# Performance work log

Measured on AMD Instinct MI355X. Metric: run time of the kernel, lower is better.

## Reference

```python
import jax, jax.numpy as jnp
import numpy as np

B, T, V, NIMG = 128, 512, 128, 1000
E, IMG_E, H = 128, 32, 1024


def setup_inputs() -> dict:
    key = jax.random.key(0)
    ks = jax.random.split(key, 10)
    s = 0.02
    input_img = jax.random.randint(ks[0], (B,), 0, NIMG)
    x = jax.random.randint(ks[1], (B, T), 0, V)
    label = jax.random.randint(ks[2], (B, T), 0, V)
    emb_img = jax.random.normal(ks[3], (NIMG, IMG_E), dtype=jnp.float32) * s
    emb_char = jax.random.normal(ks[4], (V, E), dtype=jnp.float32) * s
    emb_char = emb_char.at[0].set(0.0)  # padding_idx row zeroed, pad id = 0
    W_proj = jax.random.normal(ks[5], (E, IMG_E + E), dtype=jnp.float32) * s
    b_proj = jnp.zeros((E,), jnp.float32)
    W_ih = jax.random.normal(ks[6], (4 * H, E), dtype=jnp.float32) * s
    W_hh = jax.random.normal(ks[7], (4 * H, H), dtype=jnp.float32) * s
    b_ih = jnp.zeros((4 * H,), jnp.float32)
    b_hh = jnp.zeros((4 * H,), jnp.float32)
    W_fc = jax.random.normal(ks[8], (V, H), dtype=jnp.float32) * s
    b_fc = jnp.zeros((V,), jnp.float32)
    return dict(input_img=input_img, x=x, label=label, emb_img=emb_img,
                emb_char=emb_char, W_proj=W_proj, b_proj=b_proj,
                W_ih=W_ih, W_hh=W_hh, b_ih=b_ih, b_hh=b_hh,
                W_fc=W_fc, b_fc=b_fc)


def _forward(input_img, x, label, emb_img, emb_char, W_proj, b_proj,
             W_ih, W_hh, b_ih, b_hh, W_fc, b_fc):
    # Teacher-forced token stream: step 0 uses x[:,0], step t uses label[:,t-1]
    tok = jnp.concatenate([x[:, :1], label[:, :-1]], axis=1)          # [B,T]
    img_e = emb_img[input_img]                                        # [B,IMG_E]
    tok_e = emb_char[tok]                                             # [B,T,E]
    b, t = tok_e.shape[0], tok_e.shape[1]
    cat = jnp.concatenate(
        [jnp.broadcast_to(img_e[:, None, :], (b, t, img_e.shape[1])), tok_e],
        axis=-1)                                                      # [B,T,IMG_E+E]
    inp = jnp.einsum('btc,ec->bte', cat, W_proj) + b_proj             # [B,T,E]
    # Precompute input-to-gate projection for all timesteps (one big GEMM)
    gates_x = jnp.einsum('bte,ge->btg', inp, W_ih) + b_ih + b_hh      # [B,T,4H]
    Hh = W_hh.shape[1]

    def step(carry, gx):
        h, c = carry
        g = gx + h @ W_hh.T                                           # [B,4H]
        i, f, gg, o = jnp.split(g, 4, axis=-1)                        # torch order i,f,g,o
        c = jax.nn.sigmoid(f) * c + jax.nn.sigmoid(i) * jnp.tanh(gg)
        h = jax.nn.sigmoid(o) * jnp.tanh(c)
        return (h, c), h

    h0 = jnp.zeros((b, Hh), inp.dtype)
    (_, _), hs = jax.lax.scan(step, (h0, h0), jnp.swapaxes(gates_x, 0, 1))
    hs = jnp.swapaxes(hs, 0, 1)                                       # [B,T,H]
    logits = jnp.einsum('bth,vh->btv', hs, W_fc) + b_fc               # [B,T,V]
    return logits


def reference(input_img, x, label, emb_img, emb_char, W_proj, b_proj,
              W_ih, W_hh, b_ih, b_hh, W_fc, b_fc):
    logits = _forward(input_img, x, label, emb_img, emb_char, W_proj, b_proj,
                      W_ih, W_hh, b_ih, b_hh, W_fc, b_fc)
    preds = jnp.argmax(logits, axis=-1)                               # [B,T]
    return logits, preds
```

## Files before the change

kernel.cpp:

```cpp
#include <hip/hip_runtime.h>
#include <hip/hip_cooperative_groups.h>
#include <cmath>

#define TSTEPS 512
#define BB     128
#define HD     1024
#define GD     4096
#define VD     128
#define ED     128
#define IE     32
#define CD     160

#define DPPMOV(v, ctrl) \
    __int_as_float(__builtin_amdgcn_update_dpp(0, __float_as_int(v), (ctrl), 0xF, 0xF, true))
#define DPP_XOR7  0x141
#define DPP_XOR1  0x0B1
#define DPP_XOR2  0x04E
#define DPP_XOR8  0x128


__global__ void fold_wc_kernel(const float* __restrict__ W_ih,
                               const float* __restrict__ W_proj,
                               const float* __restrict__ b_proj,
                               const float* __restrict__ b_ih,
                               const float* __restrict__ b_hh,
                               float* __restrict__ Wc,
                               float* __restrict__ gb) {
    int idx = blockIdx.x * 256 + threadIdx.x;
    if (idx < GD * CD) {
        int g = idx / CD, c = idx - g * CD;
        const float* wr = W_ih + g * ED;
        float s = 0.f;
        #pragma unroll 8
        for (int e = 0; e < ED; ++e) s = fmaf(wr[e], W_proj[e * CD + c], s);
        Wc[idx] = s;
    }
    if (idx < GD) {
        const float* wr = W_ih + idx * ED;
        float s = b_ih[idx] + b_hh[idx];
        #pragma unroll 8
        for (int e = 0; e < ED; ++e) s = fmaf(wr[e], b_proj[e], s);
        gb[idx] = s;
    }
}

__global__ void fold_gimg_kernel(const float* __restrict__ emb_img,
                                 const int* __restrict__ input_img,
                                 const float* __restrict__ Wc,
                                 const float* __restrict__ gb,
                                 float* __restrict__ Gimgb) {
    int idx = blockIdx.x * 256 + threadIdx.x;
    int b = idx >> 12, g = idx & (GD - 1);
    const float* e = emb_img + (size_t)input_img[b] * IE;
    const float* w = Wc + g * CD;
    float s = gb[g];
    #pragma unroll
    for (int k = 0; k < IE; ++k) s = fmaf(e[k], w[k], s);
    Gimgb[idx] = s;
}

__global__ void fold_gtok_kernel(const float* __restrict__ emb_char,
                                 const float* __restrict__ Wc,
                                 float* __restrict__ Gtok) {
    int idx = blockIdx.x * 256 + threadIdx.x;
    int v = idx >> 12, g = idx & (GD - 1);
    const float* e = emb_char + v * ED;
    const float* w = Wc + g * CD + IE;
    float s = 0.f;
    #pragma unroll 8
    for (int k = 0; k < ED; ++k) s = fmaf(e[k], w[k], s);
    Gtok[idx] = s;
}

__global__ void init_kernel(const int* __restrict__ x,
                            const int* __restrict__ label,
                            int* __restrict__ tokseq,
                            float* __restrict__ hbuf,
                            unsigned* __restrict__ barcnt) {
    int idx = blockIdx.x * 256 + threadIdx.x;
    if (idx < 2 * BB * HD) hbuf[idx] = 0.f;
    if (idx < TSTEPS * BB) {
        int t = idx >> 7, b = idx & (BB - 1);
        tokseq[idx] = (t == 0) ? x[b * TSTEPS] : label[b * TSTEPS + t - 1];
    }
    if (idx < 128) barcnt[idx] = 0;
}

__global__ __launch_bounds__(1024, 4) void lstm_fused(
    const float* __restrict__ W_hh,
    const float* __restrict__ Gimgb,
    const float* __restrict__ Gtok,
    const float* __restrict__ Wfc,
    const float* __restrict__ bfc,
    const int*   __restrict__ tokseq,
    float*       __restrict__ hbuf,
    float*       __restrict__ logits,
    unsigned*    __restrict__ barcnt)
{
    __shared__ float4 hlds4[16 * 256];

    const int tid  = threadIdx.x;
    const int bid  = blockIdx.x;
    const int bgrp = bid >> 6;
    const int jgrp = bid & 63;
    const int w    = tid >> 6;
    const int L    = tid & 63;
    const int col  = jgrp * 16 + w;
    const int lrow = L & 31;
    const int row_own = bgrp * 32 + lrow;
    const int pcap = (L >> 3) & 3;
    const bool b0 = (L & 1), b1 = ((L >> 1) & 1), b2 = ((L >> 2) & 1);

    const int kc = L & 31;
    const int v  = jgrp * 2 + (L >> 5);
    const float bfcv = bfc[v];

    const float4* __restrict__ Whh4 = reinterpret_cast<const float4*>(W_hh);
    const float4* __restrict__ Wfc4 = reinterpret_cast<const float4*>(Wfc);

    float4 wreg[4][4];
    #pragma unroll
    for (int g = 0; g < 4; ++g)
        #pragma unroll
        for (int i = 0; i < 4; ++i)
            wreg[g][i] = Whh4[(size_t)(g * HD + col) * 256 + i * 64 + L];

    #pragma unroll
    for (int g = 0; g < 4; ++g)
        #pragma unroll
        for (int i = 0; i < 4; ++i)
            asm volatile("" : "+v"(wreg[g][i].x), "+v"(wreg[g][i].y),
                              "+v"(wreg[g][i].z), "+v"(wreg[g][i].w));

    unsigned* cnt = barcnt + bgrp * 32;

    float ab0, ab1, ab2, ab3;
    {
        const int tok = tokseq[row_own];
        const float* gi = Gimgb + (size_t)row_own * GD + col;
        const float* gt = Gtok  + (size_t)tok     * GD + col;
        ab0 = gi[0]    + gt[0];
        ab1 = gi[1024] + gt[1024];
        ab2 = gi[2048] + gt[2048];
        ab3 = gi[3072] + gt[3072];
    }

    float c_reg = 0.f;
    int cur = 0;

    #pragma unroll 1
    for (int t = 0; t <= TSTEPS; ++t) {
        const bool last = (t == TSTEPS);
        float aval0 = 0.f, aval1 = 0.f, aval2 = 0.f, aval3 = 0.f;

        const float4* hsrc = reinterpret_cast<const float4*>(
            hbuf + (size_t)cur * (BB * HD));

        #pragma unroll 1
        for (int st = 0; st < 2; ++st) {
            {
                const float4* src = hsrc + (size_t)(bgrp * 32 + st * 16) * 256;
                #pragma unroll
                for (int j = 0; j < 4; ++j)
                    hlds4[tid + j * 1024] = src[tid + j * 1024];
            }
            __syncthreads();

            if (t > 0) {
                float s = 0.f;
                #pragma unroll
                for (int m = 0; m < 8; ++m) {
                    float4 h4 = hlds4[w * 256 + m * 32 + kc];
                    float4 w4 = Wfc4[(size_t)v * 256 + m * 32 + kc];
                    s = fmaf(h4.x, w4.x, fmaf(h4.y, w4.y,
                        fmaf(h4.z, w4.z, fmaf(h4.w, w4.w, s))));
                }
                s += __shfl_xor(s, 1);  s += __shfl_xor(s, 2);
                s += __shfl_xor(s, 4);  s += __shfl_xor(s, 8);
                s += __shfl_xor(s, 16);
                if (kc == 0)
                    logits[((size_t)(bgrp * 32 + st * 16 + w) * TSTEPS
                            + (t - 1)) * VD + v] = s + bfcv;
            }

            if (!last) {
                #pragma unroll 1
                for (int p = 0; p < 2; ++p) {
                    float acc[4][8];
                    #pragma unroll
                    for (int g = 0; g < 4; ++g)
                        #pragma unroll
                        for (int r = 0; r < 8; ++r) acc[g][r] = 0.f;

                    #pragma unroll
                    for (int r = 0; r < 8; ++r) {
                        const int rl = p * 8 + r;
                        #pragma unroll
                        for (int i = 0; i < 4; ++i) {
                            float4 h4 = hlds4[rl * 256 + i * 64 + L];
                            #pragma unroll
                            for (int g = 0; g < 4; ++g)
                                acc[g][r] = fmaf(wreg[g][i].x, h4.x,
                                             fmaf(wreg[g][i].y, h4.y,
                                              fmaf(wreg[g][i].z, h4.z,
                                               fmaf(wreg[g][i].w, h4.w,
                                                    acc[g][r]))));
                        }
                    }

                    const bool own = (pcap == st * 2 + p);
                    #pragma unroll
                    for (int g = 0; g < 4; ++g) {
                        float m0 = b2 ? acc[g][4] : acc[g][0];
                        float s0 = b2 ? acc[g][0] : acc[g][4];
                        float m1 = b2 ? acc[g][5] : acc[g][1];
                        float s1 = b2 ? acc[g][1] : acc[g][5];
                        float m2 = b2 ? acc[g][6] : acc[g][2];
                        float s2 = b2 ? acc[g][2] : acc[g][6];
                        float m3 = b2 ? acc[g][7] : acc[g][3];
                        float s3 = b2 ? acc[g][3] : acc[g][7];
                        float n0 = m0 + DPPMOV(s0, DPP_XOR7);
                        float n1 = m1 + DPPMOV(s1, DPP_XOR7);
                        float n2 = m2 + DPPMOV(s2, DPP_XOR7);
                        float n3 = m3 + DPPMOV(s3, DPP_XOR7);
                        float p0k = b0 ? n1 : n0;
                        float p0s = b0 ? n0 : n1;
                        float p1k = b0 ? n3 : n2;
                        float p1s = b0 ? n2 : n3;
                        float q0 = p0k + DPPMOV(p0s, DPP_XOR1);
                        float q1 = p1k + DPPMOV(p1s, DPP_XOR1);
                        float rk = b1 ? q1 : q0;
                        float rs = b1 ? q0 : q1;
                        float u  = rk + DPPMOV(rs, DPP_XOR2);
                        u += DPPMOV(u, DPP_XOR8);
                        u += __int_as_float(__builtin_amdgcn_ds_swizzle(
                                 __float_as_int(u), 0x401F));
                        u += __shfl_xor(u, 32);
                        if (g == 0)      aval0 = own ? u : aval0;
                        else if (g == 1) aval1 = own ? u : aval1;
                        else if (g == 2) aval2 = own ? u : aval2;
                        else             aval3 = own ? u : aval3;
                    }
                }
            }
            __syncthreads();
        }

        if (!last) {
            float a0 = aval0 + ab0, a1 = aval1 + ab1;
            float a2 = aval2 + ab2, a3 = aval3 + ab3;
            float ig = 1.f / (1.f + expf(-a0));
            float fg = 1.f / (1.f + expf(-a1));
            float gg = tanhf(a2);
            float og = 1.f / (1.f + expf(-a3));
            c_reg = fmaf(fg, c_reg, ig * gg);
            float hnew = og * tanhf(c_reg);
            if (L < 32)
                hbuf[(size_t)(cur ^ 1) * (BB * HD)
                     + (size_t)row_own * HD + col] = hnew;

            if (t + 1 < TSTEPS) {
                const int tok = tokseq[(t + 1) * BB + row_own];
                const float* gi = Gimgb + (size_t)row_own * GD + col;
                const float* gt = Gtok  + (size_t)tok     * GD + col;
                ab0 = gi[0]    + gt[0];
                ab1 = gi[1024] + gt[1024];
                ab2 = gi[2048] + gt[2048];
                ab3 = gi[3072] + gt[3072];
            }

            __syncthreads();
            if (tid == 0) {
                __hip_atomic_fetch_add(cnt, 1u, __ATOMIC_RELEASE,
                                       __HIP_MEMORY_SCOPE_AGENT);
                const unsigned target = 64u * (unsigned)(t + 1);
                while (__hip_atomic_load(cnt, __ATOMIC_ACQUIRE,
                                         __HIP_MEMORY_SCOPE_AGENT) < target)
                    __builtin_amdgcn_s_sleep(1);
            }
            __syncthreads();
            cur ^= 1;
        }
    }
}

__global__ void argmax_kernel(const float* __restrict__ logits,
                              float* __restrict__ preds) {
    int row = blockIdx.x * 4 + (threadIdx.x >> 6);
    int lane = threadIdx.x & 63;
    const float* r = logits + (size_t)row * VD;
    float v0 = r[lane * 2], v1 = r[lane * 2 + 1];
    float bv; int bi;
    if (v1 > v0) { bv = v1; bi = lane * 2 + 1; } else { bv = v0; bi = lane * 2; }
    #pragma unroll
    for (int d = 32; d >= 1; d >>= 1) {
        float ov = __shfl_down(bv, d);
        int   oi = __shfl_down(bi, d);
        if (ov > bv || (ov == bv && oi < bi)) { bv = ov; bi = oi; }
    }
    if (lane == 0) preds[row] = (float)bi;
}

extern "C" void kernel_launch(void* const* d_in, const int* in_sizes, int n_in,
                              void* d_out, int out_size, void* d_ws, size_t ws_size,
                              hipStream_t stream) {
    const int*   input_img = (const int*)  d_in[0];
    const int*   x         = (const int*)  d_in[1];
    const int*   label     = (const int*)  d_in[2];
    const float* emb_img   = (const float*)d_in[3];
    const float* emb_char  = (const float*)d_in[4];
    const float* W_proj    = (const float*)d_in[5];
    const float* b_proj    = (const float*)d_in[6];
    const float* W_ih      = (const float*)d_in[7];
    const float* W_hh      = (const float*)d_in[8];
    const float* b_ih      = (const float*)d_in[9];
    const float* b_hh      = (const float*)d_in[10];
    const float* W_fc      = (const float*)d_in[11];
    const float* b_fc      = (const float*)d_in[12];

    float* ws      = (float*)d_ws;
    float* Wc      = ws;
    float* gb      = Wc + (size_t)GD * CD;
    float* Gimgb   = gb + GD;
    float* Gtok    = Gimgb + (size_t)BB * GD;
    float* hbuf    = Gtok + (size_t)VD * GD;
    int*   tokseq  = (int*)(hbuf + 2 * (size_t)BB * HD);
    unsigned* barcnt = (unsigned*)(tokseq + TSTEPS * BB);

    float* logits = (float*)d_out;
    float* preds  = logits + (size_t)BB * TSTEPS * VD;

    fold_wc_kernel  <<<(GD * CD + 255) / 256, 256, 0, stream>>>(W_ih, W_proj, b_proj, b_ih, b_hh, Wc, gb);
    fold_gimg_kernel<<<(BB * GD) / 256, 256, 0, stream>>>(emb_img, input_img, Wc, gb, Gimgb);
    fold_gtok_kernel<<<(VD * GD) / 256, 256, 0, stream>>>(emb_char, Wc, Gtok);
    init_kernel     <<<1024, 256, 0, stream>>>(x, label, tokseq, hbuf, barcnt);

    void* kargs[] = { (void*)&W_hh, (void*)&Gimgb, (void*)&Gtok, (void*)&W_fc,
                      (void*)&b_fc, (void*)&tokseq, (void*)&hbuf, (void*)&logits,
                      (void*)&barcnt };
    hipLaunchCooperativeKernel((void*)lstm_fused, dim3(256), dim3(1024), kargs, 0, stream);

    argmax_kernel<<<(BB * TSTEPS) / 4, 256, 0, stream>>>(logits, preds);
}
```

Baseline: 20.86 ms.

## Repartition LSTM grid to 2x128 blocks and use per-block flag barrier

Reshapes the persistent LSTM kernel from 4 batch groups of 64 blocks (1024 threads) to 2 batch groups of 128 blocks (512 threads), so each block owns 8 hidden columns over 64 batch rows. The single atomic counter barrier is replaced by per-block padded flags that each block stores, with 64 lanes polling all 128 flags of the group. The aim is to remove contention on one atomic counter and change the split of work between blocks. In exchange each block stages twice as many h rows into LDS per step, and the barrier now spans 128 blocks instead of 64.

```diff
diff --git a/kernel.cpp b/kernel.cpp
--- a/kernel.cpp
+++ b/kernel.cpp
@@ -76,17 +76,17 @@
                             const int* __restrict__ label,
                             int* __restrict__ tokseq,
                             float* __restrict__ hbuf,
-                            unsigned* __restrict__ barcnt) {
+                            unsigned* __restrict__ barflags) {
     int idx = blockIdx.x * 256 + threadIdx.x;
     if (idx < 2 * BB * HD) hbuf[idx] = 0.f;
     if (idx < TSTEPS * BB) {
         int t = idx >> 7, b = idx & (BB - 1);
         tokseq[idx] = (t == 0) ? x[b * TSTEPS] : label[b * TSTEPS + t - 1];
     }
-    if (idx < 128) barcnt[idx] = 0;
-}
-
-__global__ __launch_bounds__(1024, 4) void lstm_fused(
+    if (idx < 2 * 128 * 16) barflags[idx] = 0;
+}
+
+__global__ __launch_bounds__(512, 1) void lstm_fused(
     const float* __restrict__ W_hh,
     const float* __restrict__ Gimgb,
     const float* __restrict__ Gtok,
@@ -95,25 +95,24 @@
     const int*   __restrict__ tokseq,
     float*       __restrict__ hbuf,
     float*       __restrict__ logits,
-    unsigned*    __restrict__ barcnt)
+    unsigned*    __restrict__ barflags)
 {
     __shared__ float4 hlds4[16 * 256];
 
     const int tid  = threadIdx.x;
     const int bid  = blockIdx.x;
-    const int bgrp = bid >> 6;
-    const int jgrp = bid & 63;
+    const int bgrp = bid >> 7;
+    const int jgrp = bid & 127;
     const int w    = tid >> 6;
     const int L    = tid & 63;
-    const int col  = jgrp * 16 + w;
-    const int lrow = L & 31;
-    const int row_own = bgrp * 32 + lrow;
-    const int pcap = (L >> 3) & 3;
+    const int col  = jgrp * 8 + w;
+    const int row_own = bgrp * 64 + L;
+    const int pcap = L >> 3;
     const bool b0 = (L & 1), b1 = ((L >> 1) & 1), b2 = ((L >> 2) & 1);
 
-    const int kc = L & 31;
-    const int v  = jgrp * 2 + (L >> 5);
-    const float bfcv = bfc[v];
+    const int dotid = tid >> 5;
+    const int kc    = tid & 31;
+    const float bfcv = bfc[jgrp];
 
     const float4* __restrict__ Whh4 = reinterpret_cast<const float4*>(W_hh);
     const float4* __restrict__ Wfc4 = reinterpret_cast<const float4*>(Wfc);
@@ -132,7 +131,7 @@
             asm volatile("" : "+v"(wreg[g][i].x), "+v"(wreg[g][i].y),
                               "+v"(wreg[g][i].z), "+v"(wreg[g][i].w));
 
-    unsigned* cnt = barcnt + bgrp * 32;
+    unsigned* grpflags = barflags + bgrp * 128 * 16;
 
     float ab0, ab1, ab2, ab3;
     {
@@ -157,12 +156,12 @@
             hbuf + (size_t)cur * (BB * HD));
 
         #pragma unroll 1
-        for (int st = 0; st < 2; ++st) {
+        for (int st = 0; st < 4; ++st) {
             {
-                const float4* src = hsrc + (size_t)(bgrp * 32 + st * 16) * 256;
+                const float4* src = hsrc + (size_t)(bgrp * 64 + st * 16) * 256;
                 #pragma unroll
-                for (int j = 0; j < 4; ++j)
-                    hlds4[tid + j * 1024] = src[tid + j * 1024];
+                for (int j = 0; j < 8; ++j)
+                    hlds4[tid + j * 512] = src[tid + j * 512];
             }
             __syncthreads();
 
@@ -170,8 +169,8 @@
                 float s = 0.f;
                 #pragma unroll
                 for (int m = 0; m < 8; ++m) {
-                    float4 h4 = hlds4[w * 256 + m * 32 + kc];
-                    float4 w4 = Wfc4[(size_t)v * 256 + m * 32 + kc];
+                    float4 h4 = hlds4[dotid * 256 + m * 32 + kc];
+                    float4 w4 = Wfc4[(size_t)jgrp * 256 + m * 32 + kc];
                     s = fmaf(h4.x, w4.x, fmaf(h4.y, w4.y,
                         fmaf(h4.z, w4.z, fmaf(h4.w, w4.w, s))));
                 }
@@ -179,8 +178,8 @@
                 s += __shfl_xor(s, 4);  s += __shfl_xor(s, 8);
                 s += __shfl_xor(s, 16);
                 if (kc == 0)
-                    logits[((size_t)(bgrp * 32 + st * 16 + w) * TSTEPS
-                            + (t - 1)) * VD + v] = s + bfcv;
+                    logits[((size_t)(bgrp * 64 + st * 16 + dotid) * TSTEPS
+                            + (t - 1)) * VD + jgrp] = s + bfcv;
             }
 
             if (!last) {
@@ -255,9 +254,8 @@
             float og = 1.f / (1.f + expf(-a3));
             c_reg = fmaf(fg, c_reg, ig * gg);
             float hnew = og * tanhf(c_reg);
-            if (L < 32)
-                hbuf[(size_t)(cur ^ 1) * (BB * HD)
-                     + (size_t)row_own * HD + col] = hnew;
+            hbuf[(size_t)(cur ^ 1) * (BB * HD)
+                 + (size_t)row_own * HD + col] = hnew;
 
             if (t + 1 < TSTEPS) {
                 const int tok = tokseq[(t + 1) * BB + row_own];
@@ -270,13 +268,19 @@
             }
 
             __syncthreads();
-            if (tid == 0) {
-                __hip_atomic_fetch_add(cnt, 1u, __ATOMIC_RELEASE,
-                                       __HIP_MEMORY_SCOPE_AGENT);
-                const unsigned target = 64u * (unsigned)(t + 1);
-                while (__hip_atomic_load(cnt, __ATOMIC_ACQUIRE,
-                                         __HIP_MEMORY_SCOPE_AGENT) < target)
+            if (tid == 0)
+                __hip_atomic_store(&grpflags[jgrp * 16], (unsigned)(t + 1),
+                                   __ATOMIC_RELEASE, __HIP_MEMORY_SCOPE_AGENT);
+            if (tid < 64) {
+                const unsigned target = (unsigned)(t + 1);
+                for (;;) {
+                    unsigned fa = __hip_atomic_load(&grpflags[tid * 16],
+                                      __ATOMIC_ACQUIRE, __HIP_MEMORY_SCOPE_AGENT);
+                    unsigned fb = __hip_atomic_load(&grpflags[(64 + tid) * 16],
+                                      __ATOMIC_ACQUIRE, __HIP_MEMORY_SCOPE_AGENT);
+                    if (__all(fa >= target && fb >= target)) break;
                     __builtin_amdgcn_s_sleep(1);
+                }
             }
             __syncthreads();
             cur ^= 1;
@@ -325,7 +329,7 @@
     float* Gtok    = Gimgb + (size_t)BB * GD;
     float* hbuf    = Gtok + (size_t)VD * GD;
     int*   tokseq  = (int*)(hbuf + 2 * (size_t)BB * HD);
-    unsigned* barcnt = (unsigned*)(tokseq + TSTEPS * BB);
+    unsigned* barflags = (unsigned*)(tokseq + TSTEPS * BB);
 
     float* logits = (float*)d_out;
     float* preds  = logits + (size_t)BB * TSTEPS * VD;
@@ -333,12 +337,12 @@
     fold_wc_kernel  <<<(GD * CD + 255) / 256, 256, 0, stream>>>(W_ih, W_proj, b_proj, b_ih, b_hh, Wc, gb);
     fold_gimg_kernel<<<(BB * GD) / 256, 256, 0, stream>>>(emb_img, input_img, Wc, gb, Gimgb);
     fold_gtok_kernel<<<(VD * GD) / 256, 256, 0, stream>>>(emb_char, Wc, Gtok);
-    init_kernel     <<<1024, 256, 0, stream>>>(x, label, tokseq, hbuf, barcnt);
+    init_kernel     <<<1024, 256, 0, stream>>>(x, label, tokseq, hbuf, barflags);
 
     void* kargs[] = { (void*)&W_hh, (void*)&Gimgb, (void*)&Gtok, (void*)&W_fc,
                       (void*)&b_fc, (void*)&tokseq, (void*)&hbuf, (void*)&logits,
-                      (void*)&barcnt };
-    hipLaunchCooperativeKernel((void*)lstm_fused, dim3(256), dim3(1024), kargs, 0, stream);
+                      (void*)&barflags };
+    hipLaunchCooperativeKernel((void*)lstm_fused, dim3(256), dim3(512), kargs, 0, stream);
 
     argmax_kernel<<<(BB * TSTEPS) / 4, 256, 0, stream>>>(logits, preds);
 }
```

After: 29.18 ms. +39.9%, slower.
